# Kernel optimization log

Hardware: AMD Instinct MI355X
Metric: run time of the kernel (lower is better)

The kernel has to match this reference:

```python
import jax, jax.numpy as jnp
import numpy as np

B, T, E, H = 8, 2048, 1024, 64  # batch, seq_len(=block_size), embedding_size, head_size


def setup_inputs() -> dict:
    key = jax.random.key(0)
    k1, k2, k3, k4, k5 = jax.random.split(key, 5)
    x = jax.random.normal(k1, (B, T, E), dtype=jnp.float32)
    Wk = jax.random.normal(k2, (H, E), dtype=jnp.float32) * 0.02
    Wq = jax.random.normal(k3, (H, E), dtype=jnp.float32) * 0.02
    Wv = jax.random.normal(k4, (H, E), dtype=jnp.float32) * 0.02
    attention_mask = jax.random.randint(k5, (B, T), 0, 2).astype(jnp.int32)
    return {"x": x, "Wk": Wk, "Wq": Wq, "Wv": Wv, "attention_mask": attention_mask}


def reference(x, Wk, Wq, Wv, attention_mask):
    # Linear projections (nn.Linear with no bias: y = x @ W.T)
    k = jnp.einsum('bte,he->bth', x, Wk)
    q = jnp.einsum('bte,he->bth', x, Wq)
    v = jnp.einsum('bte,he->bth', x, Wv)
    scale = v.shape[2] ** -0.5  # head_size^-0.5, faithful to v.shape[2]**(-0.5)
    wei = jnp.einsum('bqh,bkh->bqk', q, k) * scale  # [B,T,T]
    # Causal mask (tril buffer) AND padding outer-product mask; the double-precision
    # outer product in the original just tests nonzero-ness, so a boolean AND is exact.
    causal = jnp.tril(jnp.ones((T, T), dtype=bool))  # [T,T]
    pad = (attention_mask[:, :, None] * attention_mask[:, None, :]) != 0  # [B,T,T]
    wei = jnp.where(causal[None, :, :] & pad, wei, -jnp.inf)
    wei = jax.nn.softmax(wei, axis=-1)
    wei = jnp.nan_to_num(wei)  # fully-masked rows -> 0 (matches torch.nan_to_num)
    # dropout in eval mode -> identity
    out = jnp.einsum('bqk,bkh->bqh', wei, v)
    return out
```

## Files before the change

kernel.cpp:

```cpp
#include <hip/hip_runtime.h>
#include <hip/hip_bf16.h>

typedef __bf16 bf16x8 __attribute__((ext_vector_type(8)));
typedef __bf16 bf16x4 __attribute__((ext_vector_type(4)));
typedef float  f32x4  __attribute__((ext_vector_type(4)));

#define LDP  72
#define KLDP 72
#define VLDP 72
#define PLDP 72

#define BAR() { asm volatile("s_waitcnt lgkmcnt(0)" ::: "memory"); __builtin_amdgcn_s_barrier(); }

__global__ __launch_bounds__(256) void wconv_kernel(
    const float* __restrict__ Wk, const float* __restrict__ Wq,
    const float* __restrict__ Wv, const int* __restrict__ mask,
    __bf16* __restrict__ wbf, unsigned* __restrict__ maskw)
{
    if (blockIdx.x == 192) {
        for (int wdx = threadIdx.x; wdx < 512; wdx += 256) {
            unsigned wv = 0;
            #pragma unroll
            for (int bit = 0; bit < 32; bit++)
                wv |= (mask[wdx * 32 + bit] != 0 ? 1u : 0u) << bit;
            maskw[wdx] = wv;
        }
        return;
    }
    int idx = blockIdx.x * 256 + threadIdx.x;
    int row = idx >> 8;
    int c4  = idx & 255;
    const float* wp = (row < 64) ? Wk + (size_t)row * 1024
                    : (row < 128) ? Wq + (size_t)(row - 64) * 1024
                                  : Wv + (size_t)(row - 128) * 1024;
    float4 f = *reinterpret_cast<const float4*>(wp + c4 * 4);
    bf16x4 v; v[0] = (__bf16)f.x; v[1] = (__bf16)f.y; v[2] = (__bf16)f.z; v[3] = (__bf16)f.w;
    *reinterpret_cast<bf16x4*>(&wbf[(size_t)row * 1024 + c4 * 4]) = v;
}

__global__ __launch_bounds__(512) void proj_kernel(
    const float* __restrict__ x, const __bf16* __restrict__ wbf,
    __bf16* __restrict__ kbuf, __bf16* __restrict__ qbuf, __bf16* __restrict__ vtbuf)
{
    __shared__ __align__(16) __bf16 Slds[2][256 * LDP];
    __shared__ __align__(16) __bf16 Vtl[64 * LDP];

    const int tid  = threadIdx.x;
    const int lane = tid & 63;
    const int wid  = tid >> 6;
    const int wm   = wid >> 2;
    const int wn   = wid & 3;
    const int mbase = blockIdx.x * 64;

    const int cl = lane & 15;
    const int e0 = (lane >> 4) * 8;
    const int r0 = (lane >> 4) * 4;

    const int arow = tid >> 3, acg = tid & 7;
    const float* aptr = x + (size_t)(mbase + arow) * 1024 + acg * 8;

    float4 a0a, a0b, a1a, a1b;
    bf16x8 w0[3], w1[3];

#define ISSUE(aA, aB, wset, kb) { \
    aA = *reinterpret_cast<const float4*>(aptr + (kb)); \
    aB = *reinterpret_cast<const float4*>(aptr + (kb) + 4); \
    _Pragma("unroll") \
    for (int i_ = 0; i_ < 3; i_++) { \
        int c_ = i_ * 512 + tid; \
        wset[i_] = *reinterpret_cast<const bf16x8*>(&wbf[(size_t)(c_ >> 3) * 1024 + (kb) + (c_ & 7) * 8]); \
    } }

#define COMMIT(aA, aB, wset, bufi) { \
    bf16x8 av_; \
    av_[0] = (__bf16)aA.x; av_[1] = (__bf16)aA.y; av_[2] = (__bf16)aA.z; av_[3] = (__bf16)aA.w; \
    av_[4] = (__bf16)aB.x; av_[5] = (__bf16)aB.y; av_[6] = (__bf16)aB.z; av_[7] = (__bf16)aB.w; \
    *reinterpret_cast<bf16x8*>(&Slds[bufi][arow * LDP + acg * 8]) = av_; \
    _Pragma("unroll") \
    for (int i_ = 0; i_ < 3; i_++) { \
        int c_ = i_ * 512 + tid; \
        *reinterpret_cast<bf16x8*>(&Slds[bufi][(64 + (c_ >> 3)) * LDP + (c_ & 7) * 8]) = wset[i_]; \
    } }

    f32x4 acc[2][3];
    #pragma unroll
    for (int m2 = 0; m2 < 2; m2++)
        #pragma unroll
        for (int nf = 0; nf < 3; nf++) acc[m2][nf] = (f32x4){0.f, 0.f, 0.f, 0.f};

    ISSUE(a0a, a0b, w0, 0);
    COMMIT(a0a, a0b, w0, 0);
    ISSUE(a1a, a1b, w1, 64);
    BAR();

    #pragma unroll 2
    for (int j = 0; j < 16; j++) {
        if (j < 14) {
            if (j & 1) { ISSUE(a1a, a1b, w1, (j + 2) * 64); }
            else       { ISSUE(a0a, a0b, w0, (j + 2) * 64); }
        }
        const __bf16* buf = Slds[j & 1];
        #pragma unroll
        for (int kk = 0; kk < 2; kk++) {
            bf16x8 a[2], b[3];
            #pragma unroll
            for (int m2 = 0; m2 < 2; m2++)
                a[m2] = *reinterpret_cast<const bf16x8*>(&buf[(wm * 32 + m2 * 16 + cl) * LDP + kk * 32 + e0]);
            #pragma unroll
            for (int nf = 0; nf < 3; nf++)
                b[nf] = *reinterpret_cast<const bf16x8*>(&buf[(64 + wn * 48 + nf * 16 + cl) * LDP + kk * 32 + e0]);
            #pragma unroll
            for (int m2 = 0; m2 < 2; m2++)
                #pragma unroll
                for (int nf = 0; nf < 3; nf++)
                    acc[m2][nf] = __builtin_amdgcn_mfma_f32_16x16x32_bf16(a[m2], b[nf], acc[m2][nf], 0, 0, 0);
        }
        if (j < 15) {
            if (j & 1) { COMMIT(a0a, a0b, w0, 0); }
            else       { COMMIT(a1a, a1b, w1, 1); }
            BAR();
        }
    }
#undef ISSUE
#undef COMMIT

    #pragma unroll
    for (int m2 = 0; m2 < 2; m2++)
        #pragma unroll
        for (int nf = 0; nf < 3; nf++) {
            int c = wn * 48 + nf * 16 + cl;
            #pragma unroll
            for (int r = 0; r < 4; r++) {
                int mrel = wm * 32 + m2 * 16 + r0 + r;
                float v = acc[m2][nf][r];
                if (c < 64)        kbuf[(size_t)(mbase + mrel) * 64 + c]         = (__bf16)v;
                else if (c < 128)  qbuf[(size_t)(mbase + mrel) * 64 + (c - 64)]  = (__bf16)v;
                else               Vtl[(c - 128) * LDP + mrel]                   = (__bf16)v;
            }
        }
    __syncthreads();
    {
        int b   = mbase >> 11;
        int tof = mbase & 2047;
        int h   = tid >> 3;
        int seg = tid & 7;
        bf16x8 v8 = *reinterpret_cast<const bf16x8*>(&Vtl[h * LDP + seg * 8]);
        *reinterpret_cast<bf16x8*>(&vtbuf[(size_t)b * 64 * 2048 + (size_t)h * 2048 + tof + seg * 8]) = v8;
    }
}

__global__ __launch_bounds__(256) void attn_kernel(
    const __bf16* __restrict__ qbuf, const __bf16* __restrict__ kbuf,
    const __bf16* __restrict__ vtbuf, const unsigned* __restrict__ maskw,
    float* __restrict__ out, __bf16* __restrict__ accpart, float* __restrict__ mlpart,
    int nsplit, int tps)
{
    __shared__ __align__(16) __bf16 Klds[64 * KLDP];
    __shared__ __align__(16) __bf16 Vlds[64 * VLDP];
    __shared__ __align__(16) __bf16 Plds[4][2][16 * PLDP];

    const int tid  = threadIdx.x;
    const int lane = tid & 63;
    const int w    = tid >> 6;
    const int wg   = blockIdx.x;
    const int b    = wg & 7;
    const int rr_  = wg >> 3;
    const int qt   = rr_ & 15;
    const int sp   = rr_ >> 4;

    const int jbeg = sp * tps;
    const int jend = min((sp + 1) * tps, 2 * qt + 2);

    if (nsplit > 1 && jbeg >= jend) {
        for (int i = tid; i < 128; i += 256) {
            int qrow = qt * 128 + i;
            if ((maskw[b * 64 + (qrow >> 5)] >> (qrow & 31)) & 1u) {
                size_t mo = ((size_t)(b * nsplit + sp) * 2048 + qrow) * 2;
                mlpart[mo] = -INFINITY; mlpart[mo + 1] = 0.f;
            }
        }
        return;
    }

    const int cl = lane & 15;
    const int e0 = (lane >> 4) * 8;
    const int r0 = (lane >> 4) * 4;
    const int qs0 = qt * 128 + w * 16 + cl;
    const int qs1 = qs0 + 64;

    bf16x8 aq0[2], aq1[2];
    #pragma unroll
    for (int kk = 0; kk < 2; kk++) {
        aq0[kk] = *reinterpret_cast<const bf16x8*>(&qbuf[((size_t)b * 2048 + qs0) * 64 + kk * 32 + e0]);
        aq1[kk] = *reinterpret_cast<const bf16x8*>(&qbuf[((size_t)b * 2048 + qs1) * 64 + kk * 32 + e0]);
    }

    float m0 = -INFINITY, l0 = 0.f, m1 = -INFINITY, l1 = 0.f;
    f32x4 acc0[4], acc1[4];
    #pragma unroll
    for (int hf = 0; hf < 4; hf++) { acc0[hf] = (f32x4){0.f,0.f,0.f,0.f}; acc1[hf] = (f32x4){0.f,0.f,0.f,0.f}; }

    const __bf16* kb  = kbuf  + (size_t)b * 2048 * 64;
    const __bf16* vtb = vtbuf + (size_t)b * 64 * 2048;

    const int srow = tid >> 2;
    const int sc   = (tid & 3) * 16;
    bf16x8 stk[2], stv[2];

#define KV_ISSUE(jj) { _Pragma("unroll") for (int i_ = 0; i_ < 2; i_++) { \
    stk[i_] = *reinterpret_cast<const bf16x8*>(&kb[(size_t)((jj) * 64 + srow) * 64 + sc + i_ * 8]); \
    stv[i_] = *reinterpret_cast<const bf16x8*>(&vtb[(size_t)srow * 2048 + (jj) * 64 + sc + i_ * 8]); } }

#define KV_COMMIT() { _Pragma("unroll") for (int i_ = 0; i_ < 2; i_++) { \
    *reinterpret_cast<bf16x8*>(&Klds[srow * KLDP + sc + i_ * 8]) = stk[i_]; \
    *reinterpret_cast<bf16x8*>(&Vlds[srow * VLDP + sc + i_ * 8]) = stv[i_]; } }

#define SOFTMAX(S, mS, lS, accS, qsS, su) { \
    float tmax = -INFINITY; \
    _Pragma("unroll") for (int jf = 0; jf < 4; jf++) { \
        unsigned mw = (jf < 2) ? mw0 : mw1; \
        _Pragma("unroll") for (int r = 0; r < 4; r++) { \
            int kvl = jf * 16 + r0 + r; \
            bool ok = ((mw >> (kvl & 31)) & 1u) && (j * 64 + kvl <= qsS); \
            float sv = S[jf][r] * 0.125f; \
            sv = ok ? sv : -INFINITY; \
            S[jf][r] = sv; tmax = fmaxf(tmax, sv); } } \
    tmax = fmaxf(tmax, __shfl_xor(tmax, 16)); \
    tmax = fmaxf(tmax, __shfl_xor(tmax, 32)); \
    if (!__all(tmax <= mS + 8.f)) { \
        float mn = fmaxf(mS, tmax); \
        float alpha = __expf(mS - mn); \
        lS *= alpha; mS = mn; \
        _Pragma("unroll") for (int hf = 0; hf < 4; hf++) \
            _Pragma("unroll") for (int r = 0; r < 4; r++) accS[hf][r] *= alpha; \
    } \
    float rs = 0.f; \
    _Pragma("unroll") for (int jf = 0; jf < 4; jf++) \
        _Pragma("unroll") for (int r = 0; r < 4; r++) { \
            float p = (mS == -INFINITY) ? 0.f : __expf(S[jf][r] - mS); \
            S[jf][r] = p; rs += p; } \
    rs += __shfl_xor(rs, 16); \
    rs += __shfl_xor(rs, 32); \
    lS += rs; \
    _Pragma("unroll") for (int jf = 0; jf < 4; jf++) { \
        bf16x4 p4; \
        _Pragma("unroll") for (int r = 0; r < 4; r++) p4[r] = (__bf16)S[jf][r]; \
        *reinterpret_cast<bf16x4*>(&Plds[w][su][cl * PLDP + jf * 16 + r0]) = p4; } }

    const int nt = jend - jbeg;
    KV_ISSUE(jbeg);
    KV_COMMIT();
    if (nt > 1) KV_ISSUE(jbeg + 1);
    BAR();

    for (int t = 0; t < nt; t++) {
        const int j = jbeg + t;

        f32x4 s0[4], s1[4];
        __builtin_amdgcn_s_setprio(1);
        #pragma unroll
        for (int jf = 0; jf < 4; jf++) {
            f32x4 t0 = (f32x4){0.f,0.f,0.f,0.f}, t1 = (f32x4){0.f,0.f,0.f,0.f};
            #pragma unroll
            for (int kk = 0; kk < 2; kk++) {
                bf16x8 bk = *reinterpret_cast<const bf16x8*>(&Klds[(jf * 16 + cl) * KLDP + kk * 32 + e0]);
                t0 = __builtin_amdgcn_mfma_f32_16x16x32_bf16(bk, aq0[kk], t0, 0, 0, 0);
                t1 = __builtin_amdgcn_mfma_f32_16x16x32_bf16(bk, aq1[kk], t1, 0, 0, 0);
            }
            s0[jf] = t0; s1[jf] = t1;
        }
        __builtin_amdgcn_s_setprio(0);

        const unsigned mw0 = maskw[b * 64 + j * 2];
        const unsigned mw1 = maskw[b * 64 + j * 2 + 1];
        SOFTMAX(s0, m0, l0, acc0, qs0, 0);
        SOFTMAX(s1, m1, l1, acc1, qs1, 1);

        __builtin_amdgcn_s_setprio(1);
        #pragma unroll
        for (int kk = 0; kk < 2; kk++) {
            bf16x8 p0 = *reinterpret_cast<const bf16x8*>(&Plds[w][0][cl * PLDP + kk * 32 + e0]);
            bf16x8 p1 = *reinterpret_cast<const bf16x8*>(&Plds[w][1][cl * PLDP + kk * 32 + e0]);
            #pragma unroll
            for (int hf = 0; hf < 4; hf++) {
                bf16x8 av = *reinterpret_cast<const bf16x8*>(&Vlds[(hf * 16 + cl) * VLDP + kk * 32 + e0]);
                acc0[hf] = __builtin_amdgcn_mfma_f32_16x16x32_bf16(av, p0, acc0[hf], 0, 0, 0);
                acc1[hf] = __builtin_amdgcn_mfma_f32_16x16x32_bf16(av, p1, acc1[hf], 0, 0, 0);
            }
        }
        __builtin_amdgcn_s_setprio(0);

        BAR();
        if (t + 1 < nt) {
            KV_COMMIT();
            if (t + 2 < nt) KV_ISSUE(j + 2);
            BAR();
        }
    }
#undef KV_ISSUE
#undef KV_COMMIT
#undef SOFTMAX

    const bool mq0 = (maskw[b * 64 + (qs0 >> 5)] >> (qs0 & 31)) & 1u;
    const bool mq1 = (maskw[b * 64 + (qs1 >> 5)] >> (qs1 & 31)) & 1u;
    if (nsplit == 1) {
        #pragma unroll
        for (int hf = 0; hf < 4; hf++)
            #pragma unroll
            for (int r = 0; r < 4; r++) {
                float v0 = (l0 > 0.f && mq0) ? acc0[hf][r] / l0 : 0.f;
                float v1 = (l1 > 0.f && mq1) ? acc1[hf][r] / l1 : 0.f;
                out[((size_t)b * 2048 + qs0) * 64 + hf * 16 + r0 + r] = v0;
                out[((size_t)b * 2048 + qs1) * 64 + hf * 16 + r0 + r] = v1;
            }
    } else {
        if (mq0) {
            #pragma unroll
            for (int hf = 0; hf < 4; hf++) {
                bf16x4 p4;
                #pragma unroll
                for (int r = 0; r < 4; r++) p4[r] = (__bf16)acc0[hf][r];
                *reinterpret_cast<bf16x4*>(&accpart[((size_t)(b * nsplit + sp) * 2048 + qs0) * 64 + hf * 16 + r0]) = p4;
            }
        }
        if (mq1) {
            #pragma unroll
            for (int hf = 0; hf < 4; hf++) {
                bf16x4 p4;
                #pragma unroll
                for (int r = 0; r < 4; r++) p4[r] = (__bf16)acc1[hf][r];
                *reinterpret_cast<bf16x4*>(&accpart[((size_t)(b * nsplit + sp) * 2048 + qs1) * 64 + hf * 16 + r0]) = p4;
            }
        }
        if (lane < 16) {
            if (mq0) {
                size_t mo0 = ((size_t)(b * nsplit + sp) * 2048 + qs0) * 2;
                mlpart[mo0] = m0; mlpart[mo0 + 1] = l0;
            }
            if (mq1) {
                size_t mo1 = ((size_t)(b * nsplit + sp) * 2048 + qs1) * 2;
                mlpart[mo1] = m1; mlpart[mo1 + 1] = l1;
            }
        }
    }
}

template<int NS>
__global__ __launch_bounds__(256) void combine_kernel(
    const __bf16* __restrict__ accpart, const float* __restrict__ mlpart,
    const unsigned* __restrict__ maskw, float* __restrict__ out)
{
    int idx = blockIdx.x * 256 + threadIdx.x;
    int qglob = idx >> 4;
    int h4 = (idx & 15) * 4;
    int b = qglob >> 11;
    int qrow = qglob & 2047;

    float4 o = {0.f, 0.f, 0.f, 0.f};
    if (!((maskw[b * 64 + (qrow >> 5)] >> (qrow & 31)) & 1u)) {
        *reinterpret_cast<float4*>(&out[(size_t)qglob * 64 + h4]) = o;
        return;
    }

    float m_s[NS], l_s[NS];
    float M = -INFINITY;
    #pragma unroll
    for (int s = 0; s < NS; s++) {
        size_t mo = ((size_t)(b * NS + s) * 2048 + qrow) * 2;
        m_s[s] = mlpart[mo];
        l_s[s] = mlpart[mo + 1];
        M = fmaxf(M, m_s[s]);
    }
    if (M == -INFINITY) {
        *reinterpret_cast<float4*>(&out[(size_t)qglob * 64 + h4]) = o;
        return;
    }

    float L = 0.f;
    float O0 = 0.f, O1 = 0.f, O2 = 0.f, O3 = 0.f;
    #pragma unroll
    for (int s = 0; s < NS; s++) {
        if (m_s[s] > -INFINITY) {
            float wgt = __expf(m_s[s] - M);
            L += l_s[s] * wgt;
            bf16x4 a = *reinterpret_cast<const bf16x4*>(
                &accpart[((size_t)(b * NS + s) * 2048 + qrow) * 64 + h4]);
            O0 += wgt * (float)a[0];
            O1 += wgt * (float)a[1];
            O2 += wgt * (float)a[2];
            O3 += wgt * (float)a[3];
        }
    }
    if (L > 0.f) { o.x = O0 / L; o.y = O1 / L; o.z = O2 / L; o.w = O3 / L; }
    *reinterpret_cast<float4*>(&out[(size_t)qglob * 64 + h4]) = o;
}

extern "C" void kernel_launch(void* const* d_in, const int* in_sizes, int n_in,
                              void* d_out, int out_size, void* d_ws, size_t ws_size,
                              hipStream_t stream) {
    const float* x  = (const float*)d_in[0];
    const float* Wk = (const float*)d_in[1];
    const float* Wq = (const float*)d_in[2];
    const float* Wv = (const float*)d_in[3];
    const int* mask = (const int*)d_in[4];
    float* out = (float*)d_out;

    const size_t NTOK = 8 * 2048;
    __bf16* kbuf  = (__bf16*)d_ws;
    __bf16* qbuf  = kbuf + NTOK * 64;
    __bf16* vtbuf = qbuf + NTOK * 64;
    __bf16* wbf   = vtbuf + (size_t)8 * 64 * 2048;
    unsigned* maskw = (unsigned*)(wbf + (size_t)192 * 1024);
    const size_t base_bytes = NTOK * 64 * 2 * 2 + (size_t)8 * 64 * 2048 * 2
                            + (size_t)192 * 1024 * 2 + 512 * 4;

    const size_t acc_per_split = NTOK * 64 * 2;
    const size_t ml_per_split  = NTOK * 2 * 4;
    int nsplit = 1;
    if (ws_size >= base_bytes + 4 * (acc_per_split + ml_per_split))      nsplit = 4;
    else if (ws_size >= base_bytes + 2 * (acc_per_split + ml_per_split)) nsplit = 2;

    __bf16* accpart = (__bf16*)((char*)d_ws + base_bytes);
    float*  mlpart  = (float*)(accpart + NTOK * 64 * nsplit);

    wconv_kernel<<<193, 256, 0, stream>>>(Wk, Wq, Wv, mask, wbf, maskw);
    proj_kernel<<<256, 512, 0, stream>>>(x, wbf, kbuf, qbuf, vtbuf);
    attn_kernel<<<8 * 16 * nsplit, 256, 0, stream>>>(
        qbuf, kbuf, vtbuf, maskw, out, accpart, mlpart, nsplit, 32 / nsplit);
    if (nsplit == 4)
        combine_kernel<4><<<(16384 * 16) / 256, 256, 0, stream>>>(accpart, mlpart, maskw, out);
    else if (nsplit == 2)
        combine_kernel<2><<<(16384 * 16) / 256, 256, 0, stream>>>(accpart, mlpart, maskw, out);
}
```

Before: 53.86 us.

## Load projection weights directly into LDS with XOR-swizzled layout

The weight tiles in the projection GEMM are now fetched with global_load_lds, which writes straight into shared memory instead of going through registers. Weights get their own double-buffered LDS array with an XOR swizzle to avoid bank conflicts, and the barrier waits now use explicit vmcnt counts to track the async loads. This is meant to cut register pressure and VGPR-to-LDS copy instructions in the main loop. In exchange it relies on hand-tuned waitcnt accounting, which is fragile if the compiler reorders or adds memory ops.

New measurement: 58.23 us. 1.08x slower.

```diff
diff --git a/kernel.cpp b/kernel.cpp
--- a/kernel.cpp
+++ b/kernel.cpp
@@ -42,7 +42,8 @@
     const float* __restrict__ x, const __bf16* __restrict__ wbf,
     __bf16* __restrict__ kbuf, __bf16* __restrict__ qbuf, __bf16* __restrict__ vtbuf)
 {
-    __shared__ __align__(16) __bf16 Slds[2][256 * LDP];
+    __shared__ __align__(16) __bf16 Alds[2][64 * LDP];
+    __shared__ __align__(16) __bf16 Wlds[2][192 * 64];
     __shared__ __align__(16) __bf16 Vtl[64 * LDP];
 
     const int tid  = threadIdx.x;
@@ -52,34 +53,36 @@
     const int wn   = wid & 3;
     const int mbase = blockIdx.x * 64;
 
-    const int cl = lane & 15;
-    const int e0 = (lane >> 4) * 8;
-    const int r0 = (lane >> 4) * 4;
+    const int cl  = lane & 15;
+    const int hi4 = lane >> 4;
+    const int e0  = hi4 * 8;
+    const int r0  = hi4 * 4;
 
     const int arow = tid >> 3, acg = tid & 7;
     const float* aptr = x + (size_t)(mbase + arow) * 1024 + acg * 8;
 
+    const int wrow = (tid >> 3) + 0;
     float4 a0a, a0b, a1a, a1b;
-    bf16x8 w0[3], w1[3];
-
-#define ISSUE(aA, aB, wset, kb) { \
+
+#define ISSUE_A(aA, aB, kb) { \
     aA = *reinterpret_cast<const float4*>(aptr + (kb)); \
-    aB = *reinterpret_cast<const float4*>(aptr + (kb) + 4); \
-    _Pragma("unroll") \
-    for (int i_ = 0; i_ < 3; i_++) { \
-        int c_ = i_ * 512 + tid; \
-        wset[i_] = *reinterpret_cast<const bf16x8*>(&wbf[(size_t)(c_ >> 3) * 1024 + (kb) + (c_ & 7) * 8]); \
-    } }
-
-#define COMMIT(aA, aB, wset, bufi) { \
+    aB = *reinterpret_cast<const float4*>(aptr + (kb) + 4); }
+
+#define COMMIT_A(aA, aB, bufi) { \
     bf16x8 av_; \
     av_[0] = (__bf16)aA.x; av_[1] = (__bf16)aA.y; av_[2] = (__bf16)aA.z; av_[3] = (__bf16)aA.w; \
     av_[4] = (__bf16)aB.x; av_[5] = (__bf16)aB.y; av_[6] = (__bf16)aB.z; av_[7] = (__bf16)aB.w; \
-    *reinterpret_cast<bf16x8*>(&Slds[bufi][arow * LDP + acg * 8]) = av_; \
+    *reinterpret_cast<bf16x8*>(&Alds[bufi][arow * LDP + acg * 8]) = av_; }
+
+#define W_GLOAD(kb, bufi) { \
     _Pragma("unroll") \
     for (int i_ = 0; i_ < 3; i_++) { \
-        int c_ = i_ * 512 + tid; \
-        *reinterpret_cast<bf16x8*>(&Slds[bufi][(64 + (c_ >> 3)) * LDP + (c_ & 7) * 8]) = wset[i_]; \
+        int row_ = ((i_ * 512 + tid) >> 3); \
+        const __bf16* g_ = &wbf[(size_t)row_ * 1024 + (kb) + (((tid & 7) ^ (row_ & 7)) << 3)]; \
+        __bf16* l_ = &Wlds[bufi][(size_t)(i_ * 512 + (tid & ~63)) * 8]; \
+        __builtin_amdgcn_global_load_lds( \
+            (const __attribute__((address_space(1))) void*)g_, \
+            (__attribute__((address_space(3))) void*)l_, 16, 0, 0); \
     } }
 
     f32x4 acc[2][3];
@@ -88,27 +91,33 @@
         #pragma unroll
         for (int nf = 0; nf < 3; nf++) acc[m2][nf] = (f32x4){0.f, 0.f, 0.f, 0.f};
 
-    ISSUE(a0a, a0b, w0, 0);
-    COMMIT(a0a, a0b, w0, 0);
-    ISSUE(a1a, a1b, w1, 64);
-    BAR();
+    ISSUE_A(a0a, a0b, 0);
+    COMMIT_A(a0a, a0b, 0);
+    W_GLOAD(0, 0);
+    ISSUE_A(a1a, a1b, 64);
+    asm volatile("s_waitcnt vmcnt(2) lgkmcnt(0)" ::: "memory");
+    __builtin_amdgcn_s_barrier();
 
     #pragma unroll 2
     for (int j = 0; j < 16; j++) {
+        if (j < 15) W_GLOAD((j + 1) * 64, (j & 1) ^ 1);
         if (j < 14) {
-            if (j & 1) { ISSUE(a1a, a1b, w1, (j + 2) * 64); }
-            else       { ISSUE(a0a, a0b, w0, (j + 2) * 64); }
-        }
-        const __bf16* buf = Slds[j & 1];
+            if (j & 1) { ISSUE_A(a1a, a1b, (j + 2) * 64); }
+            else       { ISSUE_A(a0a, a0b, (j + 2) * 64); }
+        }
+        const __bf16* abuf = Alds[j & 1];
+        const __bf16* wbuf = Wlds[j & 1];
         #pragma unroll
         for (int kk = 0; kk < 2; kk++) {
             bf16x8 a[2], b[3];
             #pragma unroll
             for (int m2 = 0; m2 < 2; m2++)
-                a[m2] = *reinterpret_cast<const bf16x8*>(&buf[(wm * 32 + m2 * 16 + cl) * LDP + kk * 32 + e0]);
-            #pragma unroll
-            for (int nf = 0; nf < 3; nf++)
-                b[nf] = *reinterpret_cast<const bf16x8*>(&buf[(64 + wn * 48 + nf * 16 + cl) * LDP + kk * 32 + e0]);
+                a[m2] = *reinterpret_cast<const bf16x8*>(&abuf[(wm * 32 + m2 * 16 + cl) * LDP + kk * 32 + e0]);
+            #pragma unroll
+            for (int nf = 0; nf < 3; nf++) {
+                int r = wn * 48 + nf * 16 + cl;
+                b[nf] = *reinterpret_cast<const bf16x8*>(&wbuf[r * 64 + (((kk * 4 + hi4) ^ (r & 7)) << 3)]);
+            }
             #pragma unroll
             for (int m2 = 0; m2 < 2; m2++)
                 #pragma unroll
@@ -116,13 +125,16 @@
                     acc[m2][nf] = __builtin_amdgcn_mfma_f32_16x16x32_bf16(a[m2], b[nf], acc[m2][nf], 0, 0, 0);
         }
         if (j < 15) {
-            if (j & 1) { COMMIT(a0a, a0b, w0, 0); }
-            else       { COMMIT(a1a, a1b, w1, 1); }
-            BAR();
-        }
-    }
-#undef ISSUE
-#undef COMMIT
+            if (j & 1) { COMMIT_A(a0a, a0b, 0); }
+            else       { COMMIT_A(a1a, a1b, 1); }
+            if (j < 14) { asm volatile("s_waitcnt vmcnt(2) lgkmcnt(0)" ::: "memory"); }
+            else        { asm volatile("s_waitcnt vmcnt(0) lgkmcnt(0)" ::: "memory"); }
+            __builtin_amdgcn_s_barrier();
+        }
+    }
+#undef ISSUE_A
+#undef COMMIT_A
+#undef W_GLOAD
 
     #pragma unroll
     for (int m2 = 0; m2 < 2; m2++)
```
